# Performance work log

Hardware: AMD Instinct MI355X
Metric: run time of the kernel (lower is better)

## Reference

```python
import jax, jax.numpy as jnp
import numpy as np

EPS_ROT = 1e-6
EPS_FRAME = 1e-8


def make_rotX(angs):
    # angs: [..., 2] (cos-like, sin-like); returns [..., 4, 4]
    n = jnp.sqrt(jnp.sum(angs * angs, axis=-1)) + EPS_ROT
    c = angs[..., 0] / n
    s = angs[..., 1] / n
    z = jnp.zeros_like(c)
    o = jnp.ones_like(c)
    rows = jnp.stack([o, z, z, z,
                      z, c, -s, z,
                      z, s, c, z,
                      z, z, z, o], axis=-1)
    return rows.reshape(c.shape + (4, 4))


def make_rotZ(angs):
    n = jnp.sqrt(jnp.sum(angs * angs, axis=-1)) + EPS_ROT
    c = angs[..., 0] / n
    s = angs[..., 1] / n
    z = jnp.zeros_like(c)
    o = jnp.ones_like(c)
    rows = jnp.stack([c, -s, z, z,
                      s, c, z, z,
                      z, z, o, z,
                      z, z, z, o], axis=-1)
    return rows.reshape(c.shape + (4, 4))


def make_rot_axis(angs, u):
    # Rodrigues rotation about unit axis u, as homogeneous 4x4
    n = jnp.sqrt(jnp.sum(angs * angs, axis=-1)) + EPS_ROT
    ct = angs[..., 0] / n
    st = angs[..., 1] / n
    u0, u1, u2 = u[..., 0], u[..., 1], u[..., 2]
    omc = 1.0 - ct
    z = jnp.zeros_like(ct)
    o = jnp.ones_like(ct)
    rows = jnp.stack([
        ct + u0 * u0 * omc, u0 * u1 * omc - u2 * st, u0 * u2 * omc + u1 * st, z,
        u0 * u1 * omc + u2 * st, ct + u1 * u1 * omc, u1 * u2 * omc - u0 * st, z,
        u0 * u2 * omc - u1 * st, u1 * u2 * omc + u0 * st, ct + u2 * u2 * omc, z,
        z, z, z, o], axis=-1)
    return rows.reshape(ct.shape + (4, 4))


def rigid_from_3_points(N, Ca, C):
    # Gram-Schmidt backbone frame (ideal geometry branch)
    v1 = C - Ca
    v2 = N - Ca
    e1 = v1 / (jnp.linalg.norm(v1, axis=-1, keepdims=True) + EPS_FRAME)
    u2 = v2 - e1 * jnp.sum(e1 * v2, axis=-1, keepdims=True)
    e2 = u2 / (jnp.linalg.norm(u2, axis=-1, keepdims=True) + EPS_FRAME)
    e3 = jnp.cross(e1, e2)
    R = jnp.stack([e1, e2, e3], axis=-1)  # columns -> [B,L,3,3]
    return R, Ca


def _compute(seq, xyz, alphas, base_indices, RTs_in_base_frame, xyzs_in_base_frame):
    B, L = xyz.shape[:2]
    Rs, Ts = rigid_from_3_points(xyz[..., 0, :], xyz[..., 1, :], xyz[..., 2, :])
    top = jnp.concatenate([Rs, Ts[..., None]], axis=-1)  # [B,L,3,4]
    bot = jnp.broadcast_to(jnp.array([0.0, 0.0, 0.0, 1.0], dtype=xyz.dtype), (B, L, 1, 4))
    RTF0 = jnp.concatenate([top, bot], axis=-2)  # [B,L,4,4]

    RT_base = RTs_in_base_frame[seq]  # [B,L,7,4,4]

    RTF1 = RTF0 @ RT_base[:, :, 0] @ make_rotX(alphas[:, :, 0, :])
    RTF2 = RTF0 @ RT_base[:, :, 1] @ make_rotX(alphas[:, :, 1, :])
    RTF3 = RTF0 @ RT_base[:, :, 2] @ make_rotX(alphas[:, :, 2, :])

    basexyzs = xyzs_in_base_frame[seq]  # [B,L,36,4]
    NCr = 0.5 * (basexyzs[:, :, 2, :3] + basexyzs[:, :, 0, :3])
    CAr = basexyzs[:, :, 1, :3]
    CBr = basexyzs[:, :, 4, :3]
    ax1 = jnp.cross(CBr - CAr, NCr - CAr)
    ax1 = ax1 / (jnp.linalg.norm(ax1, axis=-1, keepdims=True) + 1e-8)
    NCp = basexyzs[:, :, 2, :3] - basexyzs[:, :, 0, :3]
    NCpp = NCp - jnp.sum(NCp * NCr, axis=-1, keepdims=True) / jnp.sum(NCr * NCr, axis=-1, keepdims=True) * NCr
    ax2 = jnp.cross(CBr - CAr, NCpp)
    ax2 = ax2 / (jnp.linalg.norm(ax2, axis=-1, keepdims=True) + 1e-8)

    CBrot1 = make_rot_axis(alphas[:, :, 7, :], ax1)
    CBrot2 = make_rot_axis(alphas[:, :, 8, :], ax2)
    RTF8 = RTF0 @ CBrot1 @ CBrot2

    RTF4 = RTF8 @ RT_base[:, :, 3] @ make_rotX(alphas[:, :, 3, :]) @ make_rotZ(alphas[:, :, 9, :])
    RTF5 = RTF4 @ RT_base[:, :, 4] @ make_rotX(alphas[:, :, 4, :])
    RTF6 = RTF5 @ RT_base[:, :, 5] @ make_rotX(alphas[:, :, 5, :])
    RTF7 = RTF6 @ RT_base[:, :, 6] @ make_rotX(alphas[:, :, 6, :])

    RTframes = jnp.stack([RTF0, RTF1, RTF2, RTF3, RTF4, RTF5, RTF6, RTF7, RTF8], axis=2)  # [B,L,9,4,4]

    idx = base_indices[seq]  # [B,L,36], values in [0,9)
    frames = jnp.take_along_axis(RTframes, idx[..., None, None], axis=2)  # [B,L,36,4,4]
    xyzs = jnp.einsum('blaij,blaj->blai', frames, basexyzs)
    return RTframes, xyzs[..., :3]


def setup_inputs() -> dict:
    key = jax.random.key(0)
    ks = jax.random.split(key, 6)
    B, L, NAA, NATOMS = 4, 8192, 80, 36
    seq = jax.random.randint(ks[0], (B, L), 0, NAA)
    xyz = jax.random.normal(ks[1], (B, L, 3, 3), jnp.float32)
    alphas = jax.random.normal(ks[2], (B, L, 10, 2), jnp.float32)
    base_indices = jax.random.randint(ks[3], (NAA, NATOMS), 0, 9)
    xibf = jax.random.normal(ks[4], (NAA, NATOMS, 4), jnp.float32)
    xibf = xibf.at[..., 3].set(1.0)  # homogeneous coords
    RTs = jax.random.normal(ks[5], (NAA, 7, 4, 4), jnp.float32)
    return {"seq": seq, "xyz": xyz, "alphas": alphas, "base_indices": base_indices,
            "RTs_in_base_frame": RTs, "xyzs_in_base_frame": xibf}


def reference(seq, xyz, alphas, base_indices, RTs_in_base_frame, xyzs_in_base_frame):
    return _compute(seq, xyz, alphas, base_indices, RTs_in_base_frame, xyzs_in_base_frame)
```

## Files before the change

### kernel.cpp

```cpp
#include <hip/hip_runtime.h>

#define RPB 64
#define FRS 14
#define RSS (9*FRS)


__device__ __forceinline__ float rsqz(float d) { return rsqrtf(fmaxf(d, 1e-24f)); }

__device__ __forceinline__ void angNorm(float x, float y, float& c, float& s) {
    float inv = rsqz(x*x + y*y);
    c = x * inv; s = y * inv;
}

__device__ __forceinline__ float4 rowMat(const float4 f, const float* __restrict__ B) {
    const float4* q = reinterpret_cast<const float4*>(B);
    float4 b0 = q[0], b1 = q[1], b2 = q[2], b3 = q[3];
    float4 o;
    o.x = f.x*b0.x + f.y*b1.x + f.z*b2.x + f.w*b3.x;
    o.y = f.x*b0.y + f.y*b1.y + f.z*b2.y + f.w*b3.y;
    o.z = f.x*b0.z + f.y*b1.z + f.z*b2.z + f.w*b3.z;
    o.w = f.x*b0.w + f.y*b1.w + f.z*b2.w + f.w*b3.w;
    return o;
}

__device__ __forceinline__ void rotXrow(float4& v, float c, float s) {
    float v1 = v.y, v2 = v.z;
    v.y = c*v1 + s*v2;
    v.z = c*v2 - s*v1;
}

__device__ __forceinline__ void rotZrow(float4& v, float c, float s) {
    float v0 = v.x, v1 = v.y;
    v.x = c*v0 + s*v1;
    v.y = c*v1 - s*v0;
}

__device__ __forceinline__ float4 applyG(const float4 f, const float G[3][3]) {
    float4 o;
    o.x = f.x*G[0][0] + f.y*G[1][0] + f.z*G[2][0];
    o.y = f.x*G[0][1] + f.y*G[1][1] + f.z*G[2][1];
    o.z = f.x*G[0][2] + f.y*G[1][2] + f.z*G[2][2];
    o.w = f.w;
    return o;
}

__device__ __forceinline__ void rotAxis3(float G[3][3], float c, float s,
                                         float u0, float u1, float u2) {
    float omc = 1.0f - c;
    G[0][0] = c + u0*u0*omc;    G[0][1] = u0*u1*omc - u2*s; G[0][2] = u0*u2*omc + u1*s;
    G[1][0] = u0*u1*omc + u2*s; G[1][1] = c + u1*u1*omc;    G[1][2] = u1*u2*omc - u0*s;
    G[2][0] = u0*u2*omc - u1*s; G[2][1] = u1*u2*omc + u0*s; G[2][2] = c + u2*u2*omc;
}

__device__ __forceinline__ void ldsRow(float* fl, int frame, int i, const float4 v) {
    if (i < 3) {
        float* d = fl + frame*FRS + i*4;
        *reinterpret_cast<float2*>(d)     = make_float2(v.x, v.y);
        *reinterpret_cast<float2*>(d + 2) = make_float2(v.z, v.w);
    }
}


__global__ __launch_bounds__(256, 4) void fused_kernel(
    const int*   __restrict__ seq,
    const float* __restrict__ xyz,
    const float* __restrict__ alphas,
    const int*   __restrict__ bidx,
    const float* __restrict__ RTs,
    const float* __restrict__ xibf,
    float*       __restrict__ out_fr,
    float*       __restrict__ out_xyz,
    int BL)
{
    __shared__ __align__(16) float lds_fr[RPB * RSS];
    __shared__ int lds_seq[RPB];

    const int tid   = threadIdx.x;
    const int lane  = tid & 63;
    const int wv    = tid >> 6;
    const int i     = lane & 3;
    const int res   = wv*16 + (lane >> 2);
    const int base  = blockIdx.x * RPB;
    const int t     = base + res;
    const bool valid = (t < BL);

    float* fl = lds_fr + res * RSS;
    float* fg = out_fr + (size_t)t * 144;

    if (valid) {
        int s = seq[t];
        if (i == 0) lds_seq[res] = s;
        const float* rb = RTs + (size_t)s * 112;
        const float* al = alphas + (size_t)t * 20;

        const float* p = xyz + (size_t)t * 9;
        float N0=p[0], N1=p[1], N2=p[2];
        float A0=p[3], A1=p[4], A2=p[5];
        float C0=p[6], C1=p[7], C2=p[8];
        float v10=C0-A0, v11=C1-A1, v12=C2-A2;
        float v20=N0-A0, v21=N1-A1, v22=N2-A2;
        float i1 = rsqz(v10*v10 + v11*v11 + v12*v12);
        float e10=v10*i1, e11=v11*i1, e12=v12*i1;
        float d  = e10*v20 + e11*v21 + e12*v22;
        float u20=v20-e10*d, u21=v21-e11*d, u22=v22-e12*d;
        float i2 = rsqz(u20*u20 + u21*u21 + u22*u22);
        float e20=u20*i2, e21=u21*i2, e22=u22*i2;
        float e30=e11*e22 - e12*e21;
        float e31=e12*e20 - e10*e22;
        float e32=e10*e21 - e11*e20;

        bool c0 = (i==0), c1 = (i==1), c2 = (i==2);
        float4 f0r;
        f0r.x = c0?e10 : c1?e11 : c2?e12 : 0.f;
        f0r.y = c0?e20 : c1?e21 : c2?e22 : 0.f;
        f0r.z = c0?e30 : c1?e31 : c2?e32 : 0.f;
        f0r.w = c0?A0  : c1?A1  : c2?A2  : 1.f;
        ldsRow(fl, 0, i, f0r);
        *reinterpret_cast<float4*>(fg + i*4) = f0r;

        const float4* a4p = reinterpret_cast<const float4*>(al);
        float4 q0 = a4p[0], q1 = a4p[1], q2 = a4p[2], q3 = a4p[3], q4 = a4p[4];
        float ca0,sa0, ca1,sa1, ca2,sa2, ca3,sa3, ca4,sa4;
        float ca5,sa5, ca6,sa6, ca7,sa7, ca8,sa8, ca9,sa9;
        angNorm(q0.x,q0.y, ca0,sa0);  angNorm(q0.z,q0.w, ca1,sa1);
        angNorm(q1.x,q1.y, ca2,sa2);  angNorm(q1.z,q1.w, ca3,sa3);
        angNorm(q2.x,q2.y, ca4,sa4);  angNorm(q2.z,q2.w, ca5,sa5);
        angNorm(q3.x,q3.y, ca6,sa6);  angNorm(q3.z,q3.w, ca7,sa7);
        angNorm(q4.x,q4.y, ca8,sa8);  angNorm(q4.z,q4.w, ca9,sa9);

        float4 rw;
        rw = rowMat(f0r, rb +  0); rotXrow(rw, ca0, sa0);
        ldsRow(fl, 1, i, rw);
        *reinterpret_cast<float4*>(fg + 16 + i*4) = rw;
        rw = rowMat(f0r, rb + 16); rotXrow(rw, ca1, sa1);
        ldsRow(fl, 2, i, rw);
        *reinterpret_cast<float4*>(fg + 32 + i*4) = rw;
        rw = rowMat(f0r, rb + 32); rotXrow(rw, ca2, sa2);
        ldsRow(fl, 3, i, rw);
        *reinterpret_cast<float4*>(fg + 48 + i*4) = rw;

        const float* bxp = xibf + (size_t)s * 144;
        float4 b0 = reinterpret_cast<const float4*>(bxp)[0];
        float4 b1 = reinterpret_cast<const float4*>(bxp)[1];
        float4 b2 = reinterpret_cast<const float4*>(bxp)[2];
        float4 b4 = reinterpret_cast<const float4*>(bxp)[4];

        float NCr0 = 0.5f*(b2.x + b0.x), NCr1 = 0.5f*(b2.y + b0.y), NCr2 = 0.5f*(b2.z + b0.z);
        float ba0 = b4.x - b1.x, ba1 = b4.y - b1.y, ba2 = b4.z - b1.z;
        float w0 = NCr0 - b1.x, w1 = NCr1 - b1.y, w2 = NCr2 - b1.z;
        float x10 = ba1*w2 - ba2*w1, x11 = ba2*w0 - ba0*w2, x12 = ba0*w1 - ba1*w0;
        float in1 = rsqz(x10*x10 + x11*x11 + x12*x12);
        x10 *= in1; x11 *= in1; x12 *= in1;
        float NCp0 = b2.x - b0.x, NCp1 = b2.y - b0.y, NCp2 = b2.z - b0.z;
        float dp = NCp0*NCr0 + NCp1*NCr1 + NCp2*NCr2;
        float dr = NCr0*NCr0 + NCr1*NCr1 + NCr2*NCr2;
        float sf = dp / dr;
        float g0 = NCp0 - sf*NCr0, g1 = NCp1 - sf*NCr1, g2 = NCp2 - sf*NCr2;
        float x20 = ba1*g2 - ba2*g1, x21 = ba2*g0 - ba0*g2, x22 = ba0*g1 - ba1*g0;
        float in2 = rsqz(x20*x20 + x21*x21 + x22*x22);
        x20 *= in2; x21 *= in2; x22 *= in2;

        float G1[3][3], G2[3][3];
        rotAxis3(G1, ca7, sa7, x10, x11, x12);
        rotAxis3(G2, ca8, sa8, x20, x21, x22);

        float4 f8r = applyG(applyG(f0r, G1), G2);
        ldsRow(fl, 8, i, f8r);
        *reinterpret_cast<float4*>(fg + 128 + i*4) = f8r;

        rw = rowMat(f8r, rb + 48); rotXrow(rw, ca3, sa3); rotZrow(rw, ca9, sa9);
        ldsRow(fl, 4, i, rw);
        *reinterpret_cast<float4*>(fg + 64 + i*4) = rw;
        rw = rowMat(rw, rb + 64); rotXrow(rw, ca4, sa4);
        ldsRow(fl, 5, i, rw);
        *reinterpret_cast<float4*>(fg + 80 + i*4) = rw;
        rw = rowMat(rw, rb + 80); rotXrow(rw, ca5, sa5);
        ldsRow(fl, 6, i, rw);
        *reinterpret_cast<float4*>(fg + 96 + i*4) = rw;
        rw = rowMat(rw, rb + 96); rotXrow(rw, ca6, sa6);
        ldsRow(fl, 7, i, rw);
        *reinterpret_cast<float4*>(fg + 112 + i*4) = rw;
    }

    const int wbase = wv * 16;
#pragma unroll
    for (int k = 0; k < 9; ++k) {
        int c = k*64 + lane;
        int lres = c / 36;
        int a = c - lres*36;
        int res2 = wbase + lres;
        int tt = base + res2;
        if (tt < BL) {
            int ss  = lds_seq[res2];
            int idx = bidx[ss*36 + a];
            float4 v = *reinterpret_cast<const float4*>(xibf + ((size_t)ss*36 + a)*4);
            const float* fp = lds_fr + res2*RSS + idx*FRS;
            float2 r00 = *reinterpret_cast<const float2*>(fp + 0);
            float2 r01 = *reinterpret_cast<const float2*>(fp + 2);
            float2 r10 = *reinterpret_cast<const float2*>(fp + 4);
            float2 r11 = *reinterpret_cast<const float2*>(fp + 6);
            float2 r20 = *reinterpret_cast<const float2*>(fp + 8);
            float2 r21 = *reinterpret_cast<const float2*>(fp + 10);
            size_t o = ((size_t)(base + wbase)*36 + c)*3;
            out_xyz[o+0] = r00.x*v.x + r00.y*v.y + r01.x*v.z + r01.y*v.w;
            out_xyz[o+1] = r10.x*v.x + r10.y*v.y + r11.x*v.z + r11.y*v.w;
            out_xyz[o+2] = r20.x*v.x + r20.y*v.y + r21.x*v.z + r21.y*v.w;
        }
    }
}


extern "C" void kernel_launch(void* const* d_in, const int* in_sizes, int n_in,
                              void* d_out, int out_size, void* d_ws, size_t ws_size,
                              hipStream_t stream) {
    const int*   seq    = (const int*)  d_in[0];
    const float* xyz    = (const float*)d_in[1];
    const float* alphas = (const float*)d_in[2];
    const int*   bidx   = (const int*)  d_in[3];
    const float* RTs    = (const float*)d_in[4];
    const float* xibf   = (const float*)d_in[5];
    float*       out    = (float*)d_out;

    int BL = in_sizes[0];
    float* out_xyz = out + (size_t)BL * 144;

    int blocks = (BL + RPB - 1) / RPB;
    fused_kernel<<<blocks, 256, 0, stream>>>(seq, xyz, alphas, bidx, RTs, xibf,
                                             out, out_xyz, BL);
}
```

Measured before the change: 15.02 us.

## Split residue frame chain across two lane groups with precomputed base-frame products

Each residue now gets 8 lanes instead of 4, and blocks hold 32 residues instead of 64. The low half of the lanes computes the backbone frame, frames 1–3 and frame 8. The high half forms the chain products of RTs and rotations for frames 4–7, which do not depend on frame 8, stages them in a new LDS buffer, then multiplies them by the frame-8 rows read from LDS. The goal is to shorten the serial matrix chain by reassociating it. Because both halves sit in the same wavefront, the two branches diverge and may simply run one after the other. The reassociation also adds LDS traffic, and the high half reads frame 8 from LDS without an explicit barrier.

```diff
diff --git a/kernel.cpp b/kernel.cpp
--- a/kernel.cpp
+++ b/kernel.cpp
@@ -1,8 +1,9 @@
 #include <hip/hip_runtime.h>
 
-#define RPB 64
+#define RPB 32
 #define FRS 14
 #define RSS (9*FRS)
+#define PS  68
 
 
 __device__ __forceinline__ float rsqz(float d) { return rsqrtf(fmaxf(d, 1e-24f)); }
@@ -12,9 +13,11 @@
     c = x * inv; s = y * inv;
 }
 
-__device__ __forceinline__ float4 rowMat(const float4 f, const float* __restrict__ B) {
-    const float4* q = reinterpret_cast<const float4*>(B);
-    float4 b0 = q[0], b1 = q[1], b2 = q[2], b3 = q[3];
+__device__ __forceinline__ float4 rowMat(const float4 f, const float* B) {
+    float4 b0 = *reinterpret_cast<const float4*>(B);
+    float4 b1 = *reinterpret_cast<const float4*>(B + 4);
+    float4 b2 = *reinterpret_cast<const float4*>(B + 8);
+    float4 b3 = *reinterpret_cast<const float4*>(B + 12);
     float4 o;
     o.x = f.x*b0.x + f.y*b1.x + f.z*b2.x + f.w*b3.x;
     o.y = f.x*b0.y + f.y*b1.y + f.z*b2.y + f.w*b3.y;
@@ -73,25 +76,32 @@
     int BL)
 {
     __shared__ __align__(16) float lds_fr[RPB * RSS];
+    __shared__ __align__(16) float lds_P [RPB * PS];
     __shared__ int lds_seq[RPB];
 
-    const int tid   = threadIdx.x;
-    const int lane  = tid & 63;
-    const int wv    = tid >> 6;
-    const int i     = lane & 3;
-    const int res   = wv*16 + (lane >> 2);
-    const int base  = blockIdx.x * RPB;
-    const int t     = base + res;
+    const int tid  = threadIdx.x;
+    const int lane = tid & 63;
+    const int wv   = tid >> 6;
+    const int u    = lane & 7;
+    const int g    = lane >> 3;
+    const int i    = u & 3;
+    const bool low = (u < 4);
+    const int res  = wv*8 + g;
+    const int base = blockIdx.x * RPB;
+    const int t    = base + res;
     const bool valid = (t < BL);
 
     float* fl = lds_fr + res * RSS;
+    float* pl = lds_P  + res * PS;
     float* fg = out_fr + (size_t)t * 144;
 
-    if (valid) {
-        int s = seq[t];
-        if (i == 0) lds_seq[res] = s;
-        const float* rb = RTs + (size_t)s * 112;
-        const float* al = alphas + (size_t)t * 20;
+    int s = 0;
+    if (valid) s = seq[t];
+    const float* rb = RTs + (size_t)s * 112;
+    const float* al = alphas + (size_t)t * 20;
+
+    if (valid && low) {
+        if (u == 0) lds_seq[res] = s;
 
         const float* p = xyz + (size_t)t * 9;
         float N0=p[0], N1=p[1], N2=p[2];
@@ -118,15 +128,17 @@
         ldsRow(fl, 0, i, f0r);
         *reinterpret_cast<float4*>(fg + i*4) = f0r;
 
-        const float4* a4p = reinterpret_cast<const float4*>(al);
-        float4 q0 = a4p[0], q1 = a4p[1], q2 = a4p[2], q3 = a4p[3], q4 = a4p[4];
-        float ca0,sa0, ca1,sa1, ca2,sa2, ca3,sa3, ca4,sa4;
-        float ca5,sa5, ca6,sa6, ca7,sa7, ca8,sa8, ca9,sa9;
-        angNorm(q0.x,q0.y, ca0,sa0);  angNorm(q0.z,q0.w, ca1,sa1);
-        angNorm(q1.x,q1.y, ca2,sa2);  angNorm(q1.z,q1.w, ca3,sa3);
-        angNorm(q2.x,q2.y, ca4,sa4);  angNorm(q2.z,q2.w, ca5,sa5);
-        angNorm(q3.x,q3.y, ca6,sa6);  angNorm(q3.z,q3.w, ca7,sa7);
-        angNorm(q4.x,q4.y, ca8,sa8);  angNorm(q4.z,q4.w, ca9,sa9);
+        float2 A0p = *reinterpret_cast<const float2*>(al + 0);
+        float2 A1p = *reinterpret_cast<const float2*>(al + 2);
+        float2 A2p = *reinterpret_cast<const float2*>(al + 4);
+        float2 A7p = *reinterpret_cast<const float2*>(al + 14);
+        float2 A8p = *reinterpret_cast<const float2*>(al + 16);
+        float ca0,sa0, ca1,sa1, ca2,sa2, ca7,sa7, ca8,sa8;
+        angNorm(A0p.x,A0p.y, ca0,sa0);
+        angNorm(A1p.x,A1p.y, ca1,sa1);
+        angNorm(A2p.x,A2p.y, ca2,sa2);
+        angNorm(A7p.x,A7p.y, ca7,sa7);
+        angNorm(A8p.x,A8p.y, ca8,sa8);
 
         float4 rw;
         rw = rowMat(f0r, rb +  0); rotXrow(rw, ca0, sa0);
@@ -167,44 +179,82 @@
         float4 f8r = applyG(applyG(f0r, G1), G2);
         ldsRow(fl, 8, i, f8r);
         *reinterpret_cast<float4*>(fg + 128 + i*4) = f8r;
-
-        rw = rowMat(f8r, rb + 48); rotXrow(rw, ca3, sa3); rotZrow(rw, ca9, sa9);
-        ldsRow(fl, 4, i, rw);
-        *reinterpret_cast<float4*>(fg + 64 + i*4) = rw;
-        rw = rowMat(rw, rb + 64); rotXrow(rw, ca4, sa4);
-        ldsRow(fl, 5, i, rw);
-        *reinterpret_cast<float4*>(fg + 80 + i*4) = rw;
-        rw = rowMat(rw, rb + 80); rotXrow(rw, ca5, sa5);
-        ldsRow(fl, 6, i, rw);
-        *reinterpret_cast<float4*>(fg + 96 + i*4) = rw;
-        rw = rowMat(rw, rb + 96); rotXrow(rw, ca6, sa6);
-        ldsRow(fl, 7, i, rw);
-        *reinterpret_cast<float4*>(fg + 112 + i*4) = rw;
-    }
-
-    const int wbase = wv * 16;
+    }
+
+    if (valid && !low) {
+        float2 A3p = *reinterpret_cast<const float2*>(al + 6);
+        float2 A4p = *reinterpret_cast<const float2*>(al + 8);
+        float2 A5p = *reinterpret_cast<const float2*>(al + 10);
+        float2 A6p = *reinterpret_cast<const float2*>(al + 12);
+        float2 A9p = *reinterpret_cast<const float2*>(al + 18);
+        float ca3,sa3, ca4,sa4, ca5,sa5, ca6,sa6, ca9,sa9;
+        angNorm(A3p.x,A3p.y, ca3,sa3);
+        angNorm(A4p.x,A4p.y, ca4,sa4);
+        angNorm(A5p.x,A5p.y, ca5,sa5);
+        angNorm(A6p.x,A6p.y, ca6,sa6);
+        angNorm(A9p.x,A9p.y, ca9,sa9);
+
+        float4 p4 = *reinterpret_cast<const float4*>(rb + 48 + i*4);
+        rotXrow(p4, ca3, sa3);
+        rotZrow(p4, ca9, sa9);
+        float4 p5 = rowMat(p4, rb + 64); rotXrow(p5, ca4, sa4);
+        float4 p6 = rowMat(p5, rb + 80); rotXrow(p6, ca5, sa5);
+        float4 p7 = rowMat(p6, rb + 96); rotXrow(p7, ca6, sa6);
+
+        *reinterpret_cast<float4*>(pl +  0 + i*4) = p4;
+        *reinterpret_cast<float4*>(pl + 16 + i*4) = p5;
+        *reinterpret_cast<float4*>(pl + 32 + i*4) = p6;
+        *reinterpret_cast<float4*>(pl + 48 + i*4) = p7;
+
+        float4 f8row;
+        if (i < 3) {
+            float2 a2_ = *reinterpret_cast<const float2*>(fl + 8*FRS + i*4);
+            float2 b2_ = *reinterpret_cast<const float2*>(fl + 8*FRS + i*4 + 2);
+            f8row = make_float4(a2_.x, a2_.y, b2_.x, b2_.y);
+        } else {
+            f8row = make_float4(0.f, 0.f, 0.f, 1.f);
+        }
+
+        float4 r;
+        r = rowMat(f8row, pl +  0);
+        ldsRow(fl, 4, i, r);
+        *reinterpret_cast<float4*>(fg +  64 + i*4) = r;
+        r = rowMat(f8row, pl + 16);
+        ldsRow(fl, 5, i, r);
+        *reinterpret_cast<float4*>(fg +  80 + i*4) = r;
+        r = rowMat(f8row, pl + 32);
+        ldsRow(fl, 6, i, r);
+        *reinterpret_cast<float4*>(fg +  96 + i*4) = r;
+        r = rowMat(f8row, pl + 48);
+        ldsRow(fl, 7, i, r);
+        *reinterpret_cast<float4*>(fg + 112 + i*4) = r;
+    }
+
+    const int wbase = wv * 8;
 #pragma unroll
-    for (int k = 0; k < 9; ++k) {
+    for (int k = 0; k < 5; ++k) {
         int c = k*64 + lane;
-        int lres = c / 36;
-        int a = c - lres*36;
-        int res2 = wbase + lres;
-        int tt = base + res2;
-        if (tt < BL) {
-            int ss  = lds_seq[res2];
-            int idx = bidx[ss*36 + a];
-            float4 v = *reinterpret_cast<const float4*>(xibf + ((size_t)ss*36 + a)*4);
-            const float* fp = lds_fr + res2*RSS + idx*FRS;
-            float2 r00 = *reinterpret_cast<const float2*>(fp + 0);
-            float2 r01 = *reinterpret_cast<const float2*>(fp + 2);
-            float2 r10 = *reinterpret_cast<const float2*>(fp + 4);
-            float2 r11 = *reinterpret_cast<const float2*>(fp + 6);
-            float2 r20 = *reinterpret_cast<const float2*>(fp + 8);
-            float2 r21 = *reinterpret_cast<const float2*>(fp + 10);
-            size_t o = ((size_t)(base + wbase)*36 + c)*3;
-            out_xyz[o+0] = r00.x*v.x + r00.y*v.y + r01.x*v.z + r01.y*v.w;
-            out_xyz[o+1] = r10.x*v.x + r10.y*v.y + r11.x*v.z + r11.y*v.w;
-            out_xyz[o+2] = r20.x*v.x + r20.y*v.y + r21.x*v.z + r21.y*v.w;
+        if (c < 288) {
+            int lres = c / 36;
+            int a = c - lres*36;
+            int res2 = wbase + lres;
+            int tt = base + res2;
+            if (tt < BL) {
+                int ss  = lds_seq[res2];
+                int idx = bidx[ss*36 + a];
+                float4 v = *reinterpret_cast<const float4*>(xibf + ((size_t)ss*36 + a)*4);
+                const float* fp = lds_fr + res2*RSS + idx*FRS;
+                float2 r00 = *reinterpret_cast<const float2*>(fp + 0);
+                float2 r01 = *reinterpret_cast<const float2*>(fp + 2);
+                float2 r10 = *reinterpret_cast<const float2*>(fp + 4);
+                float2 r11 = *reinterpret_cast<const float2*>(fp + 6);
+                float2 r20 = *reinterpret_cast<const float2*>(fp + 8);
+                float2 r21 = *reinterpret_cast<const float2*>(fp + 10);
+                size_t o = ((size_t)(base + wbase)*36 + c)*3;
+                out_xyz[o+0] = r00.x*v.x + r00.y*v.y + r01.x*v.z + r01.y*v.w;
+                out_xyz[o+1] = r10.x*v.x + r10.y*v.y + r11.x*v.z + r11.y*v.w;
+                out_xyz[o+2] = r20.x*v.x + r20.y*v.y + r21.x*v.z + r21.y*v.w;
+            }
         }
     }
 }
```

Result: slower. 17.30 us (+15.2%).
